# Performance work log

Measured on AMD Instinct MI355X. Metric: run time of the kernel, lower is better.

The kernel has to match this reference:

```python
import jax, jax.numpy as jnp
import numpy as np

LAMBDA_REG = 0.1


def setup_inputs() -> dict:
    key = jax.random.key(0)
    k1, k2, k3, k4 = jax.random.split(key, 4)
    B, C, D = 4096, 10000, 128
    logits = jax.random.normal(k1, (B, C), dtype=jnp.float32)
    margins = jax.random.uniform(k2, (C,), dtype=jnp.float32)
    weights = jax.random.normal(k3, (C, D), dtype=jnp.float32)
    label = jax.random.randint(k4, (B,), 0, C, dtype=jnp.int64)
    return {"logits": logits, "margins": margins, "weights": weights, "label": label}


def reference(logits, margins, weights, label):
    B, C = logits.shape
    rows = jnp.arange(B)

    # F.cross_entropy(logits, label): mean NLL of log_softmax
    logp = jax.nn.log_softmax(logits, axis=-1)
    ce = -jnp.mean(logp[rows, label])

    # margin regularization
    margin_reg = LAMBDA_REG * jnp.mean(margins)

    # intra-class angular loss
    theta_yi = jnp.arccos(jnp.clip(logits[rows, label] / LAMBDA_REG, -1.0, 1.0))
    intra_loss = jnp.mean(theta_yi) / jnp.pi

    # inter-class loss: sum_i sum_{j != y_i} acos(clamp(w_{y_i} . w_j))
    # Vectorized replacement of the O(B*C) Python double loop:
    wy = weights[label]                       # (B, D) gather of ground-truth class rows
    S = jnp.einsum('bd,cd->bc', wy, weights)  # (B, C) pairwise dot products
    A = jnp.arccos(jnp.clip(S, -1.0, 1.0))    # (B, C) angles
    inter_sum = jnp.sum(A) - jnp.sum(A[rows, label])  # exclude j == y_i terms
    inter_loss = inter_sum / (B * (C - 1) * jnp.pi)

    return ce + margin_reg + intra_loss + inter_loss
```

## Files before the change

kernel.cpp:

```cpp
#include <hip/hip_runtime.h>
#include <stdint.h>
#include <math.h>

typedef __attribute__((ext_vector_type(8))) __bf16 bf16x8;
typedef __attribute__((ext_vector_type(4))) float floatx4;

constexpr int kB = 4096;
constexpr int kC = 10000;
constexpr int kD = 128;
constexpr int kNT = 79;
constexpr int kMT = 32;
constexpr int kBricksB = kNT * 32;
constexpr int kBricksA = kMT * 32;
constexpr int kPrepBlocks = (kBricksB + kBricksA) / 4;
constexpr float kPI = 3.14159265358979323846f;
constexpr float kLambda = 0.1f;
constexpr float kInvInter = (float)(1.0 / (4096.0 * 9999.0 * 3.141592653589793));

constexpr int kCEBlocks = kB / 4;
constexpr int kMegaBlocks = kCEBlocks + kNT * kMT;

constexpr size_t kBrickBytes = (size_t)(kBricksB + kBricksA) * 1024;
constexpr int kPartMargin = 0;
constexpr int kPartCE = 1;
constexpr int kPartInter = 1 + kB;
constexpr int kNumPart = 1 + kB + kNT * kMT;

__device__ __forceinline__ float fast_acos(float x) {
    float t = fabsf(x);
    float s = sqrtf(fmaxf(1.0f - t, 0.0f));
    float p = fmaf(fmaf(fmaf(-0.0187293f, t, 0.0742610f), t, -0.2121144f),
                   t, 1.5707288f);
    float r = s * p;
    return x < 0.0f ? kPI - r : r;
}

__device__ __forceinline__ uint16_t f2bf(float f) {
    union { float f; uint32_t u; } c; c.f = f;
    uint32_t u = c.u;
    uint32_t r = (u + 0x7FFFu + ((u >> 16) & 1u)) >> 16;
    return (uint16_t)r;
}

__global__ __launch_bounds__(256) void prep_kernel(
    const float* __restrict__ W, const float* __restrict__ margins,
    const int* __restrict__ label, uint16_t* __restrict__ wsB,
    uint16_t* __restrict__ wsA, float* __restrict__ part) {
    int blk = blockIdx.x;
    if (blk < kPrepBlocks) {
        int brick = blk * 4 + (threadIdx.x >> 6);
        int lane = threadIdx.x & 63;
        bool isA = brick >= kBricksB;
        int b2 = isA ? (brick - kBricksB) : brick;
        int kk = b2 & 3;
        int rb = (b2 >> 2) & 7;
        int tile = b2 >> 5;
        int row = tile * 128 + rb * 16 + (lane & 15);
        int k = kk * 32 + (lane >> 4) * 8;
        float v[8];
        if (isA) {
            int r = label[row];
            const float* src = W + (size_t)r * kD + k;
            #pragma unroll
            for (int j = 0; j < 8; ++j) v[j] = src[j];
        } else if (row < kC) {
            const float* src = W + (size_t)row * kD + k;
            #pragma unroll
            for (int j = 0; j < 8; ++j) v[j] = src[j];
        } else {
            #pragma unroll
            for (int j = 0; j < 8; ++j) v[j] = 0.0f;
        }
        uint4 pk;
        pk.x = (uint32_t)f2bf(v[0]) | ((uint32_t)f2bf(v[1]) << 16);
        pk.y = (uint32_t)f2bf(v[2]) | ((uint32_t)f2bf(v[3]) << 16);
        pk.z = (uint32_t)f2bf(v[4]) | ((uint32_t)f2bf(v[5]) << 16);
        pk.w = (uint32_t)f2bf(v[6]) | ((uint32_t)f2bf(v[7]) << 16);
        uint4* dst = (uint4*)(isA ? wsA : wsB);
        dst[(size_t)b2 * 64 + lane] = pk;
    } else {
        float s = 0.0f;
        for (int i = threadIdx.x; i < kC; i += 256) s += margins[i];
        for (int off = 32; off; off >>= 1) s += __shfl_down(s, off);
        __shared__ float p[4];
        if ((threadIdx.x & 63) == 0) p[threadIdx.x >> 6] = s;
        __syncthreads();
        if (threadIdx.x == 0)
            part[kPartMargin] = (p[0] + p[1] + p[2] + p[3]) * (kLambda / (float)kC);
    }
}

__global__ __launch_bounds__(256) void mega_kernel(
    const float* __restrict__ logits, const int* __restrict__ label,
    const uint16_t* __restrict__ wsA, const uint16_t* __restrict__ wsB,
    float* __restrict__ part) {
    __shared__ float red[4];
    int b = blockIdx.x;
    int cb = (int)(((long long)b * kCEBlocks) / kMegaBlocks);
    bool isce = (int)(((long long)(b + 1) * kCEBlocks) / kMegaBlocks) > cb;
    int tid = threadIdx.x;
    int wave = tid >> 6, lane = tid & 63;

    if (isce) {
        int row = cb * 4 + wave;
        const float* lp = logits + (size_t)row * kC;
        const floatx4* lp4 = (const floatx4*)lp;
        int lbl = label[row];
        float z = lp[lbl];
        float s0 = 0.0f, s1 = 0.0f, s2 = 0.0f, s3 = 0.0f;
        floatx4 v[13];
        #pragma unroll
        for (int c = 0; c < 3; ++c) {
            #pragma unroll
            for (int k = 0; k < 13; ++k)
                v[k] = __builtin_nontemporal_load(&lp4[lane + (c * 13 + k) * 64]);
            #pragma unroll
            for (int k = 0; k < 13; ++k) {
                s0 += __expf(v[k].x); s1 += __expf(v[k].y);
                s2 += __expf(v[k].z); s3 += __expf(v[k].w);
            }
        }
        if (lane < kC / 4 - 39 * 64) {
            floatx4 vt = __builtin_nontemporal_load(&lp4[39 * 64 + lane]);
            s0 += __expf(vt.x); s1 += __expf(vt.y);
            s2 += __expf(vt.z); s3 += __expf(vt.w);
        }
        float s = (s0 + s1) + (s2 + s3);
        for (int off = 32; off; off >>= 1) s += __shfl_down(s, off);
        if (lane == 0) {
            float ce = __logf(s) - z;
            float intra =
                fast_acos(fminf(fmaxf(z * (1.0f / kLambda), -1.0f), 1.0f));
            part[kPartCE + row] = ce * (1.0f / kB) + intra * (1.0f / (kB * kPI));
        }
    } else {
        int ii = b - cb;
        int mt = ii / kNT;
        int nt = ii - mt * kNT;
        int wr = wave >> 1, wc = wave & 1;

        const char* gA = (const char*)wsA + (size_t)mt * 32768;
        const char* gB = (const char*)wsB + (size_t)nt * 32768;

        floatx4 zero = {0.0f, 0.0f, 0.0f, 0.0f};
        floatx4 acc[4][4];
        #pragma unroll
        for (int i = 0; i < 4; ++i)
            #pragma unroll
            for (int jj = 0; jj < 4; ++jj) acc[i][jj] = zero;

        #pragma unroll
        for (int kk = 0; kk < 4; ++kk) {
            bf16x8 a[4], bfr[4];
            #pragma unroll
            for (int i = 0; i < 4; ++i) {
                a[i] = *(const bf16x8*)(gA + ((wr * 4 + i) * 4 + kk) * 1024 +
                                        lane * 16);
                bfr[i] = *(const bf16x8*)(gB + ((wc * 4 + i) * 4 + kk) * 1024 +
                                          lane * 16);
            }
            #pragma unroll
            for (int i = 0; i < 4; ++i)
                #pragma unroll
                for (int jj = 0; jj < 4; ++jj)
                    acc[i][jj] = __builtin_amdgcn_mfma_f32_16x16x32_bf16(
                        a[i], bfr[jj], acc[i][jj], 0, 0, 0);
        }

        float local = 0.0f;
        int col0 = nt * 128 + wc * 64 + (lane & 15);
        #pragma unroll
        for (int jj = 0; jj < 4; ++jj) {
            if (col0 + jj * 16 < kC) {
                #pragma unroll
                for (int i = 0; i < 4; ++i)
                    #pragma unroll
                    for (int r = 0; r < 4; ++r)
                        local += fast_acos(
                            fminf(fmaxf(acc[i][jj][r], -1.0f), 1.0f));
            }
        }
        for (int off = 32; off; off >>= 1) local += __shfl_down(local, off);
        if (lane == 0) red[wave] = local;
        __syncthreads();
        if (tid == 0)
            part[kPartInter + ii] = (red[0] + red[1] + red[2] + red[3]) * kInvInter;
    }
}

__global__ __launch_bounds__(256) void finalize_kernel(
    const float* __restrict__ part, float* __restrict__ out, int out_size) {
    float s = 0.0f;
    for (int i = threadIdx.x; i < kNumPart; i += 256) s += part[i];
    for (int off = 32; off; off >>= 1) s += __shfl_down(s, off);
    __shared__ float p[4];
    if ((threadIdx.x & 63) == 0) p[threadIdx.x >> 6] = s;
    __syncthreads();
    if (threadIdx.x == 0) out[0] = p[0] + p[1] + p[2] + p[3];
    for (int i = 1 + threadIdx.x; i < out_size; i += 256) out[i] = 0.0f;
}

extern "C" void kernel_launch(void* const* d_in, const int* in_sizes, int n_in,
                              void* d_out, int out_size, void* d_ws, size_t ws_size,
                              hipStream_t stream) {
    const float* logits = (const float*)d_in[0];
    const float* margins = (const float*)d_in[1];
    const float* W = (const float*)d_in[2];
    const int* label = (const int*)d_in[3];
    float* out = (float*)d_out;

    uint16_t* wsB = (uint16_t*)d_ws;
    uint16_t* wsA = (uint16_t*)((char*)d_ws + (size_t)kNT * 32768);
    float* part = (float*)((char*)d_ws + kBrickBytes);

    prep_kernel<<<kPrepBlocks + 1, 256, 0, stream>>>(W, margins, label, wsB, wsA, part);
    mega_kernel<<<kMegaBlocks, 256, 0, stream>>>(logits, label, wsA, wsB, part);
    finalize_kernel<<<1, 256, 0, stream>>>(part, out, out_size);
}
```

Measured before the change: 276.9 us.

## Split fused mega kernel into separate inter and CE kernels with double-buffered loads

Splits the interleaved mega kernel into a GEMM+acos inter-class kernel and a separate cross-entropy kernel, launched back to back on the same stream. The CE kernel now double-buffers its nontemporal loads so the next chunk's loads are issued before the exp reduction of the previous chunk. This removes the branch divergence and per-block role dispatch and lets each kernel get its own register allocation, at the cost of losing overlap between the memory-bound CE work and the compute-bound GEMM work, plus one extra launch.

```diff
diff --git a/kernel.cpp b/kernel.cpp
--- a/kernel.cpp
+++ b/kernel.cpp
@@ -18,7 +18,7 @@
 constexpr float kInvInter = (float)(1.0 / (4096.0 * 9999.0 * 3.141592653589793));
 
 constexpr int kCEBlocks = kB / 4;
-constexpr int kMegaBlocks = kCEBlocks + kNT * kMT;
+constexpr int kInterBlocks = kNT * kMT;
 
 constexpr size_t kBrickBytes = (size_t)(kBricksB + kBricksA) * 1024;
 constexpr int kPartMargin = 0;
@@ -90,101 +90,114 @@
     }
 }
 
-__global__ __launch_bounds__(256) void mega_kernel(
-    const float* __restrict__ logits, const int* __restrict__ label,
+__global__ __launch_bounds__(256) void inter_kernel(
     const uint16_t* __restrict__ wsA, const uint16_t* __restrict__ wsB,
     float* __restrict__ part) {
     __shared__ float red[4];
-    int b = blockIdx.x;
-    int cb = (int)(((long long)b * kCEBlocks) / kMegaBlocks);
-    bool isce = (int)(((long long)(b + 1) * kCEBlocks) / kMegaBlocks) > cb;
+    int ii = blockIdx.x;
+    int mt = ii / kNT;
+    int nt = ii - mt * kNT;
     int tid = threadIdx.x;
     int wave = tid >> 6, lane = tid & 63;
-
-    if (isce) {
-        int row = cb * 4 + wave;
-        const float* lp = logits + (size_t)row * kC;
-        const floatx4* lp4 = (const floatx4*)lp;
-        int lbl = label[row];
-        float z = lp[lbl];
-        float s0 = 0.0f, s1 = 0.0f, s2 = 0.0f, s3 = 0.0f;
-        floatx4 v[13];
+    int wr = wave >> 1, wc = wave & 1;
+
+    const char* gA = (const char*)wsA + (size_t)mt * 32768;
+    const char* gB = (const char*)wsB + (size_t)nt * 32768;
+
+    floatx4 zero = {0.0f, 0.0f, 0.0f, 0.0f};
+    floatx4 acc[4][4];
+    #pragma unroll
+    for (int i = 0; i < 4; ++i)
         #pragma unroll
-        for (int c = 0; c < 3; ++c) {
-            #pragma unroll
-            for (int k = 0; k < 13; ++k)
-                v[k] = __builtin_nontemporal_load(&lp4[lane + (c * 13 + k) * 64]);
-            #pragma unroll
-            for (int k = 0; k < 13; ++k) {
-                s0 += __expf(v[k].x); s1 += __expf(v[k].y);
-                s2 += __expf(v[k].z); s3 += __expf(v[k].w);
-            }
+        for (int jj = 0; jj < 4; ++jj) acc[i][jj] = zero;
+
+    #pragma unroll
+    for (int kk = 0; kk < 4; ++kk) {
+        bf16x8 a[4], bfr[4];
+        #pragma unroll
+        for (int i = 0; i < 4; ++i) {
+            a[i] = *(const bf16x8*)(gA + ((wr * 4 + i) * 4 + kk) * 1024 +
+                                    lane * 16);
+            bfr[i] = *(const bf16x8*)(gB + ((wc * 4 + i) * 4 + kk) * 1024 +
+                                      lane * 16);
         }
-        if (lane < kC / 4 - 39 * 64) {
-            floatx4 vt = __builtin_nontemporal_load(&lp4[39 * 64 + lane]);
-            s0 += __expf(vt.x); s1 += __expf(vt.y);
-            s2 += __expf(vt.z); s3 += __expf(vt.w);
-        }
-        float s = (s0 + s1) + (s2 + s3);
-        for (int off = 32; off; off >>= 1) s += __shfl_down(s, off);
-        if (lane == 0) {
-            float ce = __logf(s) - z;
-            float intra =
-                fast_acos(fminf(fmaxf(z * (1.0f / kLambda), -1.0f), 1.0f));
-            part[kPartCE + row] = ce * (1.0f / kB) + intra * (1.0f / (kB * kPI));
-        }
-    } else {
-        int ii = b - cb;
-        int mt = ii / kNT;
-        int nt = ii - mt * kNT;
-        int wr = wave >> 1, wc = wave & 1;
-
-        const char* gA = (const char*)wsA + (size_t)mt * 32768;
-        const char* gB = (const char*)wsB + (size_t)nt * 32768;
-
-        floatx4 zero = {0.0f, 0.0f, 0.0f, 0.0f};
-        floatx4 acc[4][4];
         #pragma unroll
         for (int i = 0; i < 4; ++i)
             #pragma unroll
-            for (int jj = 0; jj < 4; ++jj) acc[i][jj] = zero;
-
-        #pragma unroll
-        for (int kk = 0; kk < 4; ++kk) {
-            bf16x8 a[4], bfr[4];
-            #pragma unroll
-            for (int i = 0; i < 4; ++i) {
-                a[i] = *(const bf16x8*)(gA + ((wr * 4 + i) * 4 + kk) * 1024 +
-                                        lane * 16);
-                bfr[i] = *(const bf16x8*)(gB + ((wc * 4 + i) * 4 + kk) * 1024 +
-                                          lane * 16);
-            }
+            for (int jj = 0; jj < 4; ++jj)
+                acc[i][jj] = __builtin_amdgcn_mfma_f32_16x16x32_bf16(
+                    a[i], bfr[jj], acc[i][jj], 0, 0, 0);
+    }
+
+    float local = 0.0f;
+    int col0 = nt * 128 + wc * 64 + (lane & 15);
+    #pragma unroll
+    for (int jj = 0; jj < 4; ++jj) {
+        if (col0 + jj * 16 < kC) {
             #pragma unroll
             for (int i = 0; i < 4; ++i)
                 #pragma unroll
-                for (int jj = 0; jj < 4; ++jj)
-                    acc[i][jj] = __builtin_amdgcn_mfma_f32_16x16x32_bf16(
-                        a[i], bfr[jj], acc[i][jj], 0, 0, 0);
+                for (int r = 0; r < 4; ++r)
+                    local += fast_acos(fminf(fmaxf(acc[i][jj][r], -1.0f), 1.0f));
         }
-
-        float local = 0.0f;
-        int col0 = nt * 128 + wc * 64 + (lane & 15);
-        #pragma unroll
-        for (int jj = 0; jj < 4; ++jj) {
-            if (col0 + jj * 16 < kC) {
-                #pragma unroll
-                for (int i = 0; i < 4; ++i)
-                    #pragma unroll
-                    for (int r = 0; r < 4; ++r)
-                        local += fast_acos(
-                            fminf(fmaxf(acc[i][jj][r], -1.0f), 1.0f));
-            }
-        }
-        for (int off = 32; off; off >>= 1) local += __shfl_down(local, off);
-        if (lane == 0) red[wave] = local;
-        __syncthreads();
-        if (tid == 0)
-            part[kPartInter + ii] = (red[0] + red[1] + red[2] + red[3]) * kInvInter;
+    }
+    for (int off = 32; off; off >>= 1) local += __shfl_down(local, off);
+    if (lane == 0) red[wave] = local;
+    __syncthreads();
+    if (tid == 0)
+        part[kPartInter + ii] = (red[0] + red[1] + red[2] + red[3]) * kInvInter;
+}
+
+__global__ __launch_bounds__(256) void ce_kernel(
+    const float* __restrict__ logits, const int* __restrict__ label,
+    float* __restrict__ part) {
+    int tid = threadIdx.x;
+    int wave = tid >> 6, lane = tid & 63;
+    int row = blockIdx.x * 4 + wave;
+    const float* lp = logits + (size_t)row * kC;
+    const floatx4* lp4 = (const floatx4*)lp;
+    int lbl = label[row];
+    float z = lp[lbl];
+    float s0 = 0.0f, s1 = 0.0f, s2 = 0.0f, s3 = 0.0f;
+    floatx4 v[13], w[13];
+    bool hastail = lane < kC / 4 - 39 * 64;
+    floatx4 vt;
+
+    #pragma unroll
+    for (int k = 0; k < 13; ++k)
+        v[k] = __builtin_nontemporal_load(&lp4[lane + k * 64]);
+    #pragma unroll
+    for (int k = 0; k < 13; ++k)
+        w[k] = __builtin_nontemporal_load(&lp4[lane + (13 + k) * 64]);
+    #pragma unroll
+    for (int k = 0; k < 13; ++k) {
+        s0 += __expf(v[k].x); s1 += __expf(v[k].y);
+        s2 += __expf(v[k].z); s3 += __expf(v[k].w);
+    }
+    #pragma unroll
+    for (int k = 0; k < 13; ++k)
+        v[k] = __builtin_nontemporal_load(&lp4[lane + (26 + k) * 64]);
+    #pragma unroll
+    for (int k = 0; k < 13; ++k) {
+        s0 += __expf(w[k].x); s1 += __expf(w[k].y);
+        s2 += __expf(w[k].z); s3 += __expf(w[k].w);
+    }
+    if (hastail) vt = __builtin_nontemporal_load(&lp4[39 * 64 + lane]);
+    #pragma unroll
+    for (int k = 0; k < 13; ++k) {
+        s0 += __expf(v[k].x); s1 += __expf(v[k].y);
+        s2 += __expf(v[k].z); s3 += __expf(v[k].w);
+    }
+    if (hastail) {
+        s0 += __expf(vt.x); s1 += __expf(vt.y);
+        s2 += __expf(vt.z); s3 += __expf(vt.w);
+    }
+    float s = (s0 + s1) + (s2 + s3);
+    for (int off = 32; off; off >>= 1) s += __shfl_down(s, off);
+    if (lane == 0) {
+        float ce = __logf(s) - z;
+        float intra = fast_acos(fminf(fmaxf(z * (1.0f / kLambda), -1.0f), 1.0f));
+        part[kPartCE + row] = ce * (1.0f / kB) + intra * (1.0f / (kB * kPI));
     }
 }
 
@@ -214,6 +227,7 @@
     float* part = (float*)((char*)d_ws + kBrickBytes);
 
     prep_kernel<<<kPrepBlocks + 1, 256, 0, stream>>>(W, margins, label, wsB, wsA, part);
-    mega_kernel<<<kMegaBlocks, 256, 0, stream>>>(logits, label, wsA, wsB, part);
+    inter_kernel<<<kInterBlocks, 256, 0, stream>>>(wsA, wsB, part);
+    ce_kernel<<<kCEBlocks, 256, 0, stream>>>(logits, label, part);
     finalize_kernel<<<1, 256, 0, stream>>>(part, out, out_size);
 }
```

Result: no change. 279.5 us (+0.9%).
